# Kernel optimization log

Hardware: AMD Instinct MI355X
Metric: run time of the kernel (lower is better)

The kernel has to match this reference:

```python
import jax, jax.numpy as jnp
import numpy as np

NUM_CLASSES = 5
VDIM = 16
IN_CH = 512
B, H, W = 32, 64, 64
LEVEL_OFFSETS = [0, 2, 5, 9]  # flat offsets of levels 1..4 (2,3,4,5 nodes)


def conv1x1(x, w, b):
    # x: [B,C,H,W], w: [O,C], b: [O] -> [B,O,H,W]
    return jnp.einsum('bchw,oc->bohw', x, w) + b[None, :, None, None]


def setup_inputs() -> dict:
    key = jax.random.key(0)
    ks = jax.random.split(key, 8)
    features = jax.random.normal(ks[0], (B, IN_CH, H, W), dtype=jnp.float32)
    # He init (fan_out = out_channels for 1x1 convs), biases zero
    root_w = jax.random.normal(ks[1], (VDIM, IN_CH), dtype=jnp.float32) * np.sqrt(2.0 / VDIM)
    root_b = jnp.zeros((VDIM,), jnp.float32)
    level_w = jax.random.normal(ks[2], (14, VDIM, VDIM), dtype=jnp.float32) * np.sqrt(2.0 / VDIM)
    level_b = jnp.zeros((14, VDIM), jnp.float32)
    m1_w = jax.random.normal(ks[3], (64, VDIM), dtype=jnp.float32) * np.sqrt(2.0 / 64.0)
    m1_b = jnp.zeros((64,), jnp.float32)
    m2_w = jax.random.normal(ks[4], (1, 64), dtype=jnp.float32) * np.sqrt(2.0 / 1.0)
    m2_b = jnp.zeros((1,), jnp.float32)
    return dict(features=features, root_w=root_w, root_b=root_b,
                level_w=level_w, level_b=level_b,
                m1_w=m1_w, m1_b=m1_b, m2_w=m2_w, m2_b=m2_b)


def reference(features, root_w, root_b, level_w, level_b, m1_w, m1_b, m2_w, m2_b):
    b = features.shape[0]
    feats = [conv1x1(features, root_w, root_b)]  # level 0: root, [B,VDIM,H,W]
    for level in range(1, NUM_CLASSES):
        off = LEVEL_OFFSETS[level - 1]
        num_nodes = level + 1
        nxt = []
        for node in range(num_nodes):
            pl = max(0, node - 1)
            pr = min(node, level - 1)
            if pl == pr:
                parent = feats[pl]
            else:
                # L2 norm of GAP-pooled parent vectors; pick larger-norm parent
                ln = jnp.linalg.norm(feats[pl].mean(axis=(2, 3)), axis=1)  # [B]
                rn = jnp.linalg.norm(feats[pr].mean(axis=(2, 3)), axis=1)
                sel = (rn > ln).astype(features.dtype)[:, None, None, None]
                parent = feats[pl] * (1.0 - sel) + feats[pr] * sel
            nxt.append(conv1x1(parent, level_w[off + node], level_b[off + node]))
        feats = nxt
    # leaves: NUM_CLASSES tensors [B,VDIM,H,W]
    leaf_pooled = jnp.stack([f.mean(axis=(2, 3)) for f in feats], axis=1)  # [B,K,VDIM]
    class_logits = jnp.linalg.norm(leaf_pooled, axis=2)                    # [B,K]
    selected_class = jnp.argmax(class_logits, axis=1)                      # [B]
    leaf_stack = jnp.stack(feats, axis=1)                                  # [B,K,VDIM,H,W]
    sel_idx = selected_class[:, None, None, None, None]
    selected_feat = jnp.take_along_axis(leaf_stack, sel_idx, axis=1)[:, 0]  # [B,VDIM,H,W]
    feat_norm = jnp.linalg.norm(selected_feat, axis=1, keepdims=True) + 1e-8
    normalized = selected_feat / feat_norm
    m1 = jax.nn.relu(conv1x1(normalized, m1_w, m1_b))
    m2 = conv1x1(m1, m2_w, m2_b)                 # [B,1,H,W]
    mantissa_raw = m2.mean(axis=(2, 3))[:, 0]    # [B]
    mantissa = jax.nn.sigmoid(mantissa_raw) * 0.75 + 0.75
    return (class_logits, mantissa, selected_class)
```

## Files before the change

kernel.cpp:

```cpp
#include <hip/hip_runtime.h>
#include <math.h>

#define HW 4096
#define NB 32
#define VD 16
#define CPB 128

#define OFF_M0P   0
#define OFF_MSP   8192
#define OFF_M     8448
#define OFF_C     16640
#define OFF_WT    17152
#define OFF_P     25344
#define PSZ       2097152

__global__ __launch_bounds__(256) void k_trans(const float* __restrict__ rw,
                                               float* __restrict__ wt) {
    int i = blockIdx.x * 256 + threadIdx.x;
    if (i < 512 * VD) {
        int c = i >> 4, o = i & 15;
        wt[i] = rw[o * 512 + c];
    }
}

__global__ __launch_bounds__(256) void k_root(const float* __restrict__ feat,
                                              const float* __restrict__ wt,
                                              const float* __restrict__ rb,
                                              float* __restrict__ pbase,
                                              float* __restrict__ m0p) {
    const int b  = blockIdx.y;
    const int s  = blockIdx.z;
    const int bx = blockIdx.x;
    const int t  = threadIdx.x;
    const int px = bx * 1024 + t * 4;
    const int cb = s * CPB;
    const float* fp = feat + ((size_t)b * 512 + cb) * HW + px;
    const float* wp = wt + (size_t)cb * VD;

    float4 acc[VD];
#pragma unroll
    for (int o = 0; o < VD; ++o) {
        float bb = (s == 0) ? rb[o] : 0.0f;
        acc[o].x = bb; acc[o].y = bb; acc[o].z = bb; acc[o].w = bb;
    }

    float4 cur[4], nxt[4];
#pragma unroll
    for (int k = 0; k < 4; ++k) cur[k] = *(const float4*)(fp + (size_t)k * HW);

    for (int c = 0; c < CPB; c += 4) {
        if (c + 4 < CPB) {
#pragma unroll
            for (int k = 0; k < 4; ++k)
                nxt[k] = *(const float4*)(fp + (size_t)(c + 4 + k) * HW);
        }
        const float* wr = wp + c * VD;
#pragma unroll
        for (int j = 0; j < 4; ++j) {
#pragma unroll
            for (int o = 0; o < VD; ++o) {
                float w = wr[j * VD + o];
                acc[o].x += w * cur[j].x;
                acc[o].y += w * cur[j].y;
                acc[o].z += w * cur[j].z;
                acc[o].w += w * cur[j].w;
            }
        }
#pragma unroll
        for (int k = 0; k < 4; ++k) cur[k] = nxt[k];
    }

    float* op = pbase + (size_t)s * PSZ + (size_t)b * VD * HW + px;
#pragma unroll
    for (int o = 0; o < VD; ++o) *(float4*)(op + (size_t)o * HW) = acc[o];

    __shared__ float red[4][VD];
    const int lane = t & 63, wv = t >> 6;
#pragma unroll
    for (int o = 0; o < VD; ++o) {
        float v = acc[o].x + acc[o].y + acc[o].z + acc[o].w;
#pragma unroll
        for (int off = 32; off > 0; off >>= 1) v += __shfl_down(v, off);
        if (lane == 0) red[wv][o] = v;
    }
    __syncthreads();
    if (t < VD)
        m0p[((b * 4 + s) * 4 + bx) * VD + t] =
            red[0][t] + red[1][t] + red[2][t] + red[3][t];
}

__global__ __launch_bounds__(64) void k_tree(const float* __restrict__ lw,
                                             const float* __restrict__ lb,
                                             float* __restrict__ ws,
                                             float* __restrict__ out) {
    const int b = blockIdx.x;
    const int t = threadIdx.x;
    __shared__ float lm[15][VD];
    __shared__ float Wst[256];
    __shared__ int   path[5];
    const int Soff[5] = {0, 1, 3, 6, 10};
    const int LOFF[4] = {0, 2, 5, 9};

    if (t < VD) {
        float s = 0.f;
        for (int k = 0; k < 16; ++k) s += ws[OFF_M0P + (b * 16 + k) * VD + t];
        lm[0][t] = s * (1.0f / HW);
    }
    __syncthreads();

    for (int l = 1; l <= 4; ++l) {
        if (t < VD) {
            for (int n = 0; n <= l; ++n) {
                int pl = (n - 1 < 0) ? 0 : (n - 1);
                int pr = (n < l - 1) ? n : (l - 1);
                const float* A = lm[Soff[l - 1] + pl];
                const float* R = lm[Soff[l - 1] + pr];
                bool takeR = false;
                if (pl != pr) {
                    float ln = 0.f, rn = 0.f;
                    for (int k = 0; k < VD; ++k) { ln += A[k] * A[k]; rn += R[k] * R[k]; }
                    takeR = sqrtf(rn) > sqrtf(ln);
                }
                int widx = LOFF[l - 1] + n;
                float s = lb[widx * VD + t];
                for (int k = 0; k < VD; ++k) {
                    float pk = takeR ? R[k] : A[k];
                    s += lw[(widx * VD + t) * VD + k] * pk;
                }
                lm[Soff[l] + n][t] = s;
            }
        }
        __syncthreads();
    }

    if (t == 0) {
        float best = -1.f; int bi = 0;
        for (int n = 0; n < 5; ++n) {
            float s = 0.f;
            for (int k = 0; k < VD; ++k) { float v = lm[10 + n][k]; s += v * v; }
            float lg = sqrtf(s);
            out[b * 5 + n] = lg;
            if (lg > best) { best = lg; bi = n; }
        }
        out[192 + b] = (float)bi;
        int node = bi;
        for (int l = 4; l >= 1; --l) {
            path[l] = LOFF[l - 1] + node;
            int pl = (node - 1 < 0) ? 0 : (node - 1);
            int pr = (node < l - 1) ? node : (l - 1);
            if (pl == pr) node = pl;
            else {
                float ln = 0.f, rn = 0.f;
                for (int k = 0; k < VD; ++k) {
                    float a = lm[Soff[l - 1] + pl][k], r = lm[Soff[l - 1] + pr][k];
                    ln += a * a; rn += r * r;
                }
                node = (sqrtf(rn) > sqrtf(ln)) ? pr : pl;
            }
        }
    }
    __syncthreads();

    for (int i = t; i < 256; i += 64) Wst[i] = lw[path[1] * 256 + i];
    __syncthreads();
    float Mc[VD], cc[VD];
    if (t < VD) {
        for (int i = 0; i < VD; ++i) Mc[i] = Wst[i * VD + t];
        for (int i = 0; i < VD; ++i) cc[i] = lb[path[1] * VD + i];
    }
    for (int l = 2; l <= 4; ++l) {
        __syncthreads();
        for (int i = t; i < 256; i += 64) Wst[i] = lw[path[l] * 256 + i];
        __syncthreads();
        if (t < VD) {
            float nM[VD], nc[VD];
            for (int i = 0; i < VD; ++i) {
                float sm = 0.f, sc = 0.f;
                for (int k = 0; k < VD; ++k) {
                    float w = Wst[i * VD + k];
                    sm += w * Mc[k]; sc += w * cc[k];
                }
                nM[i] = sm; nc[i] = sc + lb[path[l] * VD + i];
            }
            for (int i = 0; i < VD; ++i) { Mc[i] = nM[i]; cc[i] = nc[i]; }
        }
    }
    if (t < VD) {
        for (int i = 0; i < VD; ++i) ws[OFF_M + b * 256 + i * VD + t] = Mc[i];
        if (t == 0) for (int i = 0; i < VD; ++i) ws[OFF_C + b * VD + i] = cc[i];
    }
}

__global__ __launch_bounds__(256) void k_final(const float* __restrict__ pbase,
                                               const float* __restrict__ Mg,
                                               const float* __restrict__ Cg,
                                               const float* __restrict__ m1w,
                                               const float* __restrict__ m1b,
                                               const float* __restrict__ m2w,
                                               const float* __restrict__ m2b,
                                               float* __restrict__ msp) {
    const int b = blockIdx.y;
    const int t = threadIdx.x;
    __shared__ float sM[256], sc[VD], s1w[1024], s1b[64], s2w[64];
    sM[t] = Mg[b * 256 + t];
    for (int i = t; i < 1024; i += 256) s1w[i] = m1w[i];
    if (t < 64) { s1b[t] = m1b[t]; s2w[t] = m2w[t]; }
    if (t < VD) sc[t] = Cg[b * VD + t];
    __syncthreads();

    const size_t base = (size_t)b * VD * HW + blockIdx.x * 512 + t * 2;
    float2 f[VD];
#pragma unroll
    for (int j = 0; j < VD; ++j) {
        float2 a0 = *(const float2*)(pbase + base + (size_t)j * HW);
        float2 a1 = *(const float2*)(pbase + PSZ + base + (size_t)j * HW);
        float2 a2 = *(const float2*)(pbase + 2 * PSZ + base + (size_t)j * HW);
        float2 a3 = *(const float2*)(pbase + 3 * (size_t)PSZ + base + (size_t)j * HW);
        f[j].x = a0.x + a1.x + a2.x + a3.x;
        f[j].y = a0.y + a1.y + a2.y + a3.y;
    }

    float2 v[VD];
#pragma unroll
    for (int i = 0; i < VD; ++i) {
        float2 s; s.x = s.y = sc[i];
#pragma unroll
        for (int j = 0; j < VD; ++j) {
            float w = sM[i * VD + j];
            s.x += w * f[j].x; s.y += w * f[j].y;
        }
        v[i] = s;
    }

    float2 n2; n2.x = n2.y = 0.f;
#pragma unroll
    for (int i = 0; i < VD; ++i) { n2.x += v[i].x * v[i].x; n2.y += v[i].y * v[i].y; }
    float2 inv;
    inv.x = 1.f / (sqrtf(n2.x) + 1e-8f);
    inv.y = 1.f / (sqrtf(n2.y) + 1e-8f);
#pragma unroll
    for (int i = 0; i < VD; ++i) { v[i].x *= inv.x; v[i].y *= inv.y; }

    float mb = m2b[0];
    float2 s2; s2.x = s2.y = mb;
#pragma unroll 8
    for (int o = 0; o < 64; ++o) {
        float2 h; h.x = h.y = s1b[o];
#pragma unroll
        for (int i = 0; i < VD; ++i) {
            float w = s1w[o * VD + i];
            h.x += w * v[i].x; h.y += w * v[i].y;
        }
        h.x = fmaxf(h.x, 0.f); h.y = fmaxf(h.y, 0.f);
        float w2 = s2w[o];
        s2.x += w2 * h.x; s2.y += w2 * h.y;
    }
    float psum = s2.x + s2.y;

    const int lane = t & 63, wv = t >> 6;
#pragma unroll
    for (int off = 32; off > 0; off >>= 1) psum += __shfl_down(psum, off);
    __shared__ float rs[4];
    if (lane == 0) rs[wv] = psum;
    __syncthreads();
    if (t == 0) msp[b * 8 + blockIdx.x] = rs[0] + rs[1] + rs[2] + rs[3];
}

__global__ __launch_bounds__(64) void k_mant(const float* __restrict__ msp,
                                             float* __restrict__ out) {
    int b = threadIdx.x;
    if (b < NB) {
        float m = 0.f;
        for (int k = 0; k < 8; ++k) m += msp[b * 8 + k];
        m *= (1.0f / HW);
        out[160 + b] = (1.0f / (1.0f + expf(-m))) * 0.75f + 0.75f;
    }
}

extern "C" void kernel_launch(void* const* d_in, const int* in_sizes, int n_in,
                              void* d_out, int out_size, void* d_ws, size_t ws_size,
                              hipStream_t stream) {
    const float* feat    = (const float*)d_in[0];
    const float* root_w  = (const float*)d_in[1];
    const float* root_b  = (const float*)d_in[2];
    const float* level_w = (const float*)d_in[3];
    const float* level_b = (const float*)d_in[4];
    const float* m1w     = (const float*)d_in[5];
    const float* m1b     = (const float*)d_in[6];
    const float* m2w     = (const float*)d_in[7];
    const float* m2b     = (const float*)d_in[8];
    float* ws  = (float*)d_ws;
    float* out = (float*)d_out;

    k_trans<<<32, 256, 0, stream>>>(root_w, ws + OFF_WT);
    k_root<<<dim3(4, NB, 4), 256, 0, stream>>>(feat, ws + OFF_WT, root_b,
                                               ws + OFF_P, ws + OFF_M0P);
    k_tree<<<NB, 64, 0, stream>>>(level_w, level_b, ws, out);
    k_final<<<dim3(8, NB), 256, 0, stream>>>(ws + OFF_P, ws + OFF_M, ws + OFF_C,
                                             m1w, m1b, m2w, m2b, ws + OFF_MSP);
    k_mant<<<1, 64, 0, stream>>>(ws + OFF_MSP, out);
}
```

Measured before the change: 417.6 us.

## Split root conv into eight channel groups with whole-image blocks

The root 1x1 conv now uses 512-thread blocks that each cover the whole 4096-pixel image for a 64-channel slice. Each thread holds two float4 pixel groups and consumes two channels per step. There are now eight partial-sum buffers instead of four, so the tree and final kernels sum eight partials per pixel and per pooled mean. The aim is to reuse each weight load across more pixels and change the work split, but it doubles the partial-buffer write and read traffic, needs twice the workspace, and launches fewer, larger blocks.

```diff
diff --git a/kernel.cpp b/kernel.cpp
--- a/kernel.cpp
+++ b/kernel.cpp
@@ -4,7 +4,6 @@
 #define HW 4096
 #define NB 32
 #define VD 16
-#define CPB 128
 
 #define OFF_M0P   0
 #define OFF_MSP   8192
@@ -12,7 +11,7 @@
 #define OFF_C     16640
 #define OFF_WT    17152
 #define OFF_P     25344
-#define PSZ       2097152
+#define PB        2097152
 
 __global__ __launch_bounds__(256) void k_trans(const float* __restrict__ rw,
                                                float* __restrict__ wt) {
@@ -23,70 +22,87 @@
     }
 }
 
-__global__ __launch_bounds__(256) void k_root(const float* __restrict__ feat,
-                                              const float* __restrict__ wt,
-                                              const float* __restrict__ rb,
-                                              float* __restrict__ pbase,
-                                              float* __restrict__ m0p) {
-    const int b  = blockIdx.y;
-    const int s  = blockIdx.z;
-    const int bx = blockIdx.x;
+__global__ __launch_bounds__(512, 2) void k_root(const float* __restrict__ feat,
+                                                 const float* __restrict__ wt,
+                                                 const float* __restrict__ rb,
+                                                 float* __restrict__ pbase,
+                                                 float* __restrict__ m0p) {
+    const int b  = blockIdx.x;
+    const int g  = blockIdx.y;
     const int t  = threadIdx.x;
-    const int px = bx * 1024 + t * 4;
-    const int cb = s * CPB;
+    const int cb = g * 64;
+    const int px = t * 4;
     const float* fp = feat + ((size_t)b * 512 + cb) * HW + px;
     const float* wp = wt + (size_t)cb * VD;
 
-    float4 acc[VD];
+    float4 acc[VD][2];
 #pragma unroll
     for (int o = 0; o < VD; ++o) {
-        float bb = (s == 0) ? rb[o] : 0.0f;
-        acc[o].x = bb; acc[o].y = bb; acc[o].z = bb; acc[o].w = bb;
-    }
-
-    float4 cur[4], nxt[4];
-#pragma unroll
-    for (int k = 0; k < 4; ++k) cur[k] = *(const float4*)(fp + (size_t)k * HW);
-
-    for (int c = 0; c < CPB; c += 4) {
-        if (c + 4 < CPB) {
-#pragma unroll
-            for (int k = 0; k < 4; ++k)
-                nxt[k] = *(const float4*)(fp + (size_t)(c + 4 + k) * HW);
+        float bb = (g == 0) ? rb[o] : 0.0f;
+        acc[o][0].x = bb; acc[o][0].y = bb; acc[o][0].z = bb; acc[o][0].w = bb;
+        acc[o][1] = acc[o][0];
+    }
+
+    float4 b0[2], b1[2], t0[2], t1[2];
+    b0[0] = *(const float4*)(fp);
+    b0[1] = *(const float4*)(fp + 2048);
+    b1[0] = *(const float4*)(fp + HW);
+    b1[1] = *(const float4*)(fp + HW + 2048);
+
+    for (int c = 0; c < 64; c += 2) {
+        if (c + 2 < 64) {
+            const float* np = fp + (size_t)(c + 2) * HW;
+            t0[0] = *(const float4*)(np);
+            t0[1] = *(const float4*)(np + 2048);
+            t1[0] = *(const float4*)(np + HW);
+            t1[1] = *(const float4*)(np + HW + 2048);
         }
         const float* wr = wp + c * VD;
 #pragma unroll
-        for (int j = 0; j < 4; ++j) {
-#pragma unroll
-            for (int o = 0; o < VD; ++o) {
-                float w = wr[j * VD + o];
-                acc[o].x += w * cur[j].x;
-                acc[o].y += w * cur[j].y;
-                acc[o].z += w * cur[j].z;
-                acc[o].w += w * cur[j].w;
-            }
-        }
-#pragma unroll
-        for (int k = 0; k < 4; ++k) cur[k] = nxt[k];
-    }
-
-    float* op = pbase + (size_t)s * PSZ + (size_t)b * VD * HW + px;
-#pragma unroll
-    for (int o = 0; o < VD; ++o) *(float4*)(op + (size_t)o * HW) = acc[o];
-
-    __shared__ float red[4][VD];
+        for (int o = 0; o < VD; ++o) {
+            float w = wr[o];
+            acc[o][0].x += w * b0[0].x; acc[o][0].y += w * b0[0].y;
+            acc[o][0].z += w * b0[0].z; acc[o][0].w += w * b0[0].w;
+            acc[o][1].x += w * b0[1].x; acc[o][1].y += w * b0[1].y;
+            acc[o][1].z += w * b0[1].z; acc[o][1].w += w * b0[1].w;
+        }
+        const float* wr2 = wp + (c + 1) * VD;
+#pragma unroll
+        for (int o = 0; o < VD; ++o) {
+            float w = wr2[o];
+            acc[o][0].x += w * b1[0].x; acc[o][0].y += w * b1[0].y;
+            acc[o][0].z += w * b1[0].z; acc[o][0].w += w * b1[0].w;
+            acc[o][1].x += w * b1[1].x; acc[o][1].y += w * b1[1].y;
+            acc[o][1].z += w * b1[1].z; acc[o][1].w += w * b1[1].w;
+        }
+#pragma unroll
+        for (int k = 0; k < 2; ++k) { b0[k] = t0[k]; b1[k] = t1[k]; }
+    }
+
+    float* op = pbase + (size_t)g * PB + ((size_t)b * VD) * HW + px;
+#pragma unroll
+    for (int o = 0; o < VD; ++o) {
+        *(float4*)(op + (size_t)o * HW)        = acc[o][0];
+        *(float4*)(op + (size_t)o * HW + 2048) = acc[o][1];
+    }
+
+    __shared__ float red[8][VD];
     const int lane = t & 63, wv = t >> 6;
 #pragma unroll
     for (int o = 0; o < VD; ++o) {
-        float v = acc[o].x + acc[o].y + acc[o].z + acc[o].w;
+        float v = acc[o][0].x + acc[o][0].y + acc[o][0].z + acc[o][0].w
+                + acc[o][1].x + acc[o][1].y + acc[o][1].z + acc[o][1].w;
 #pragma unroll
         for (int off = 32; off > 0; off >>= 1) v += __shfl_down(v, off);
         if (lane == 0) red[wv][o] = v;
     }
     __syncthreads();
-    if (t < VD)
-        m0p[((b * 4 + s) * 4 + bx) * VD + t] =
-            red[0][t] + red[1][t] + red[2][t] + red[3][t];
+    if (t < VD) {
+        float s = 0.f;
+#pragma unroll
+        for (int k = 0; k < 8; ++k) s += red[k][t];
+        m0p[(b * 8 + g) * VD + t] = s;
+    }
 }
 
 __global__ __launch_bounds__(64) void k_tree(const float* __restrict__ lw,
@@ -103,7 +119,7 @@
 
     if (t < VD) {
         float s = 0.f;
-        for (int k = 0; k < 16; ++k) s += ws[OFF_M0P + (b * 16 + k) * VD + t];
+        for (int k = 0; k < 8; ++k) s += ws[OFF_M0P + (b * 8 + k) * VD + t];
         lm[0][t] = s * (1.0f / HW);
     }
     __syncthreads();
@@ -212,12 +228,13 @@
     float2 f[VD];
 #pragma unroll
     for (int j = 0; j < VD; ++j) {
-        float2 a0 = *(const float2*)(pbase + base + (size_t)j * HW);
-        float2 a1 = *(const float2*)(pbase + PSZ + base + (size_t)j * HW);
-        float2 a2 = *(const float2*)(pbase + 2 * PSZ + base + (size_t)j * HW);
-        float2 a3 = *(const float2*)(pbase + 3 * (size_t)PSZ + base + (size_t)j * HW);
-        f[j].x = a0.x + a1.x + a2.x + a3.x;
-        f[j].y = a0.y + a1.y + a2.y + a3.y;
+        float2 s; s.x = s.y = 0.f;
+#pragma unroll
+        for (int g = 0; g < 8; ++g) {
+            float2 a = *(const float2*)(pbase + (size_t)g * PB + base + (size_t)j * HW);
+            s.x += a.x; s.y += a.y;
+        }
+        f[j] = s;
     }
 
     float2 v[VD];
@@ -293,8 +310,8 @@
     float* out = (float*)d_out;
 
     k_trans<<<32, 256, 0, stream>>>(root_w, ws + OFF_WT);
-    k_root<<<dim3(4, NB, 4), 256, 0, stream>>>(feat, ws + OFF_WT, root_b,
-                                               ws + OFF_P, ws + OFF_M0P);
+    k_root<<<dim3(NB, 8), 512, 0, stream>>>(feat, ws + OFF_WT, root_b,
+                                            ws + OFF_P, ws + OFF_M0P);
     k_tree<<<NB, 64, 0, stream>>>(level_w, level_b, ws, out);
     k_final<<<dim3(8, NB), 256, 0, stream>>>(ws + OFF_P, ws + OFF_M, ws + OFF_C,
                                              m1w, m1b, m2w, m2b, ws + OFF_MSP);
```

New measurement: 441.0 us. 5.6% more time.
